# Optimization experiments

Hardware: AMD Instinct MI355X
Metric: run time of the kernel (lower is better)

## Reference

```python
import jax, jax.numpy as jnp
import numpy as np

H = 1024          # hidden_size
NH = 16           # num_attention_heads
HD = H // NH      # attention_head_size = 64
B, S = 8, 1024
LN_EPS = 1e-12


def setup_inputs() -> dict:
    key = jax.random.key(0)
    ks = jax.random.split(key, 12)
    sc = 0.02
    return {
        "input_tensor": jax.random.normal(ks[0], (B, S, H), dtype=jnp.float32),
        "attention_mask": jnp.zeros((B, S), dtype=jnp.float32),
        # LinearMem params (quantization disabled -> plain Linear, torch layout [out,in])
        "Wq": jax.random.normal(ks[1], (H, H), dtype=jnp.float32) * sc,
        "bq": jnp.zeros((H,), dtype=jnp.float32),
        "Wk": jax.random.normal(ks[2], (H, H), dtype=jnp.float32) * sc,
        "bk": jnp.zeros((H,), dtype=jnp.float32),
        "Wv": jax.random.normal(ks[3], (H, H), dtype=jnp.float32) * sc,
        "bv": jnp.zeros((H,), dtype=jnp.float32),
        "Wo": jax.random.normal(ks[4], (H, H), dtype=jnp.float32) * sc,
        "bo": jnp.zeros((H,), dtype=jnp.float32),
        "ln_gamma": jnp.ones((H,), dtype=jnp.float32),
        "ln_beta": jnp.zeros((H,), dtype=jnp.float32),
    }


def _heads(x):  # [B,S,H] -> [B,NH,S,HD]
    return x.reshape(B, S, NH, HD).transpose(0, 2, 1, 3)


def reference(input_tensor, attention_mask, Wq, bq, Wk, bk, Wv, bv, Wo, bo, ln_gamma, ln_beta):
    # Q/K/V projections (LinearMem with quantization disabled == Linear)
    q = _heads(jnp.einsum('bsh,oh->bso', input_tensor, Wq) + bq)
    k = _heads(jnp.einsum('bsh,oh->bso', input_tensor, Wk) + bk)
    v = _heads(jnp.einsum('bsh,oh->bso', input_tensor, Wv) + bv)
    scores = jnp.einsum('bnqd,bnkd->bnqk', q, k) / np.float32(np.sqrt(HD))
    scores = scores + attention_mask[:, None, None, :]  # additive mask [B,1,1,S]
    probs = jax.nn.softmax(scores, axis=-1)  # dropout = identity in eval
    ctx = jnp.einsum('bnqk,bnkd->bnqd', probs, v)
    ctx = ctx.transpose(0, 2, 1, 3).reshape(B, S, H)
    # output projection + residual LayerNorm (eps=1e-12)
    out = jnp.einsum('bsh,oh->bso', ctx, Wo) + bo
    resid = out + input_tensor
    mu = jnp.mean(resid, axis=-1, keepdims=True)
    var = jnp.mean(jnp.square(resid - mu), axis=-1, keepdims=True)
    return (resid - mu) * jax.lax.rsqrt(var + LN_EPS) * ln_gamma + ln_beta
```

## Files before the change

### kernel.cpp

```cpp
#include <hip/hip_runtime.h>

#define NHh 16

typedef unsigned short ushortT;
typedef __attribute__((ext_vector_type(8))) short short8;
typedef __attribute__((ext_vector_type(4))) float floatx4;

__device__ __forceinline__ ushortT f2bf(float x) {
    union { float f; unsigned int u; } cv; cv.f = x;
    unsigned int u = cv.u;
    unsigned int r = u + 0x7fffu + ((u >> 16) & 1u);
    return (ushortT)(r >> 16);
}

__device__ __forceinline__ unsigned pack2_trunc(float a, float b) {
    union { float f; unsigned u; } ua, ub;
    ua.f = a; ub.f = b;
    return (ub.u & 0xffff0000u) | (ua.u >> 16);
}

__device__ __forceinline__ void gload_lds16(const ushortT* g, ushortT* l) {
    __builtin_amdgcn_global_load_lds(
        (const __attribute__((address_space(1))) void*)g,
        (__attribute__((address_space(3))) void*)l, 16, 0, 0);
}

__global__ __launch_bounds__(256) void cvt_all(const float* __restrict__ x,
        const float* __restrict__ W0, const float* __restrict__ W1,
        const float* __restrict__ W2, const float* __restrict__ W3,
        ushortT* __restrict__ Xb, ushortT* __restrict__ Wall, ushortT* __restrict__ Wob) {
    int bid = blockIdx.x;
    const float* in; ushortT* out; int i;
    if (bid < 8192) {
        in = x; out = Xb; i = bid * 256 + threadIdx.x;
    } else {
        int z = (bid - 8192) >> 10;
        in = (z == 0) ? W0 : (z == 1) ? W1 : (z == 2) ? W2 : W3;
        out = (z < 3) ? (Wall + (size_t)z * 1048576) : Wob;
        i = ((bid - 8192) & 1023) * 256 + threadIdx.x;
    }
    float4 f = ((const float4*)in)[i];
    uint2 o;
    o.x = (unsigned)f2bf(f.x) | ((unsigned)f2bf(f.y) << 16);
    o.y = (unsigned)f2bf(f.z) | ((unsigned)f2bf(f.w) << 16);
    ((uint2*)out)[i] = o;
}

__global__ __launch_bounds__(512, 1) void qkv_pipe(
        const ushortT* __restrict__ X, const ushortT* __restrict__ Wall,
        const float* __restrict__ b0, const float* __restrict__ b1, const float* __restrict__ b2,
        ushortT* __restrict__ Qo, ushortT* __restrict__ Ko, ushortT* __restrict__ Vo) {
    __shared__ __align__(16) ushortT As[2 * 16384];
    __shared__ __align__(16) ushortT Bs[2 * 12288];

    const int l = blockIdx.x;
    const int xcd = l & 7;
    const int j = l >> 3;
    const int mg = j >> 4;
    const int nt = j & 15;
    const int arow0 = (mg * 8 + xcd) * 256;
    const int brow0 = nt * 192;

    const int tid = threadIdx.x;
    const int lane = tid & 63;
    const int w = tid >> 6;
    const int wr = w >> 2;
    const int wc = w & 3;
    const int qd = lane >> 4, ln = lane & 15;

    const ushortT* srcA[4]; const ushortT* srcB[3];
    int oA[4], oB[3];
#pragma unroll
    for (int k = 0; k < 4; k++) {
        int o = k * 8192 + tid * 16;
        int rowblk = o >> 11, ks = (o >> 10) & 1, r = (o >> 6) & 15;
        int c2 = ((o >> 4) & 3) ^ ((r >> 3) << 1);
        srcA[k] = X + (size_t)(arow0 + rowblk * 16 + r) * 1024 + ks * 32 + c2 * 8;
        oA[k] = o;
    }
#pragma unroll
    for (int k = 0; k < 3; k++) {
        int o = k * 8192 + tid * 16;
        int rowblk = o >> 11, ks = (o >> 10) & 1, r = (o >> 6) & 15;
        int c2 = ((o >> 4) & 3) ^ ((r >> 3) << 1);
        srcB[k] = Wall + (size_t)(brow0 + rowblk * 16 + r) * 1024 + ks * 32 + c2 * 8;
        oB[k] = o;
    }

    floatx4 acc[8][3];
#pragma unroll
    for (int i = 0; i < 8; i++)
#pragma unroll
        for (int jj = 0; jj < 3; jj++) acc[i][jj] = (floatx4){0.f, 0.f, 0.f, 0.f};

    auto STAGE = [&](int buf) {
#pragma unroll
        for (int k = 0; k < 4; k++) {
            gload_lds16(srcA[k], (ushortT*)((char*)As + buf * 32768 + oA[k]));
            srcA[k] += 64;
        }
#pragma unroll
        for (int k = 0; k < 3; k++) {
            gload_lds16(srcB[k], (ushortT*)((char*)Bs + buf * 24576 + oB[k]));
            srcB[k] += 64;
        }
    };

    const int lnc = ln * 64 + ((qd ^ ((ln >> 3) << 1)) * 16);

    short8 a0[8], bf0[3], a1[8], bf1[3];

    auto RD = [&](short8 (&af)[8], short8 (&bf)[3], const char* Ab, const char* Bb, int ksb) {
#pragma unroll
        for (int mi = 0; mi < 8; mi++)
            af[mi] = *(const short8*)(Ab + (wr * 8 + mi) * 2048 + ksb + lnc);
#pragma unroll
        for (int ni = 0; ni < 3; ni++)
            bf[ni] = *(const short8*)(Bb + (wc * 3 + ni) * 2048 + ksb + lnc);
    };
    auto MM = [&](short8 (&af)[8], short8 (&bf)[3]) {
        __builtin_amdgcn_s_setprio(1);
#pragma unroll
        for (int mi = 0; mi < 8; mi++)
#pragma unroll
            for (int ni = 0; ni < 3; ni++)
                acc[mi][ni] = __builtin_amdgcn_mfma_f32_16x16x32_bf16(af[mi], bf[ni], acc[mi][ni], 0, 0, 0);
        __builtin_amdgcn_s_setprio(0);
    };

    STAGE(0); STAGE(1);
    asm volatile("s_waitcnt vmcnt(7)" ::: "memory");
    __builtin_amdgcn_s_barrier();
    RD(a0, bf0, (const char*)As, (const char*)Bs, 0);
    asm volatile("s_waitcnt lgkmcnt(0)" ::: "memory");
    __builtin_amdgcn_sched_barrier(0);

    for (int T = 0; T < 16; T++) {
        const char* Ab = (const char*)As + (T & 1) * 32768;
        const char* Bb = (const char*)Bs + (T & 1) * 24576;
        const char* An = (const char*)As + ((T + 1) & 1) * 32768;
        const char* Bn = (const char*)Bs + ((T + 1) & 1) * 24576;
        RD(a1, bf1, Ab, Bb, 1024);
        __builtin_amdgcn_sched_barrier(0);
        MM(a0, bf0);
        asm volatile("s_waitcnt lgkmcnt(0)" ::: "memory");
        asm volatile("s_waitcnt vmcnt(0)" ::: "memory");
        __builtin_amdgcn_sched_barrier(0);
        __builtin_amdgcn_s_barrier();
        if (T < 14) STAGE(T & 1);
        if (T < 15) RD(a0, bf0, An, Bn, 0);
        __builtin_amdgcn_sched_barrier(0);
        MM(a1, bf1);
        asm volatile("s_waitcnt lgkmcnt(0)" ::: "memory");
        __builtin_amdgcn_sched_barrier(0);
    }

#pragma unroll
    for (int ni = 0; ni < 3; ni++) {
        int n = brow0 + wc * 48 + ni * 16 + ln;
        int z = n >> 10;
        int col = n & 1023;
        int h = col >> 6, d = col & 63;
        const float* bias = (z == 0) ? b0 : (z == 1) ? b1 : b2;
        float bb = bias[col];
        if (z == 2) {
#pragma unroll
            for (int mi = 0; mi < 8; mi++) {
                int m = arow0 + wr * 128 + mi * 16 + qd * 4;
                int b = m >> 10, s = m & 1023;
                ushort4 pk;
                pk.x = f2bf(acc[mi][ni][0] + bb);
                pk.y = f2bf(acc[mi][ni][1] + bb);
                pk.z = f2bf(acc[mi][ni][2] + bb);
                pk.w = f2bf(acc[mi][ni][3] + bb);
                *(ushort4*)&Vo[((size_t)(b * NHh + h) * 64 + d) * 1024 + s] = pk;
            }
        } else {
            ushortT* Out = z ? Ko : Qo;
#pragma unroll
            for (int mi = 0; mi < 8; mi++) {
#pragma unroll
                for (int r2 = 0; r2 < 4; r2++) {
                    int m = arow0 + wr * 128 + mi * 16 + qd * 4 + r2;
                    int b = m >> 10, s = m & 1023;
                    Out[(size_t)((b * NHh + h) * 1024 + s) * 64 + d] =
                        f2bf(acc[mi][ni][r2] + bb);
                }
            }
        }
    }
}

__device__ __forceinline__ void gemm_core_256x128(
        const ushortT* __restrict__ Ap, const ushortT* __restrict__ Bp,
        int arow0, int brow0, ushortT* As3, ushortT* Bs3,
        int tid, int wr, int wc, int qd, int ln, floatx4 (&acc)[4][4]) {
    const ushortT* srcA[4]; const ushortT* srcB[2];
    int oA[4], oB[2];
#pragma unroll
    for (int k = 0; k < 4; k++) {
        int o = k * 8192 + tid * 16;
        int rowblk = o >> 11, ks = (o >> 10) & 1, r = (o >> 6) & 15;
        int c2 = ((o >> 4) & 3) ^ ((r >> 3) << 1);
        srcA[k] = Ap + (size_t)(arow0 + rowblk * 16 + r) * 1024 + ks * 32 + c2 * 8;
        oA[k] = o;
    }
#pragma unroll
    for (int k = 0; k < 2; k++) {
        int o = k * 8192 + tid * 16;
        int rowblk = o >> 11, ks = (o >> 10) & 1, r = (o >> 6) & 15;
        int c2 = ((o >> 4) & 3) ^ ((r >> 3) << 1);
        srcB[k] = Bp + (size_t)(brow0 + rowblk * 16 + r) * 1024 + ks * 32 + c2 * 8;
        oB[k] = o;
    }
#pragma unroll
    for (int t = 0; t < 2; t++) {
#pragma unroll
        for (int k = 0; k < 4; k++) {
            gload_lds16(srcA[k], (ushortT*)((char*)As3 + t * 32768 + oA[k]));
            srcA[k] += 64;
        }
#pragma unroll
        for (int k = 0; k < 2; k++) {
            gload_lds16(srcB[k], (ushortT*)((char*)Bs3 + t * 16384 + oB[k]));
            srcB[k] += 64;
        }
    }
    asm volatile("s_waitcnt vmcnt(6)" ::: "memory");
    __builtin_amdgcn_s_barrier();

    const int lnc = ln * 64 + ((qd ^ ((ln >> 3) << 1)) * 16);

    int bi = 0, si = 2;
    for (int T = 0; T < 16; T++) {
        const char* Ab = (const char*)As3 + bi * 32768;
        const char* Bb = (const char*)Bs3 + bi * 16384;
        short8 afr[4][2], bfr[4][2];
#pragma unroll
        for (int mi = 0; mi < 4; mi++)
#pragma unroll
            for (int ks = 0; ks < 2; ks++)
                afr[mi][ks] = *(const short8*)(Ab + (mi * 4 + wr) * 2048 + ks * 1024 + lnc);
#pragma unroll
        for (int ni = 0; ni < 4; ni++)
#pragma unroll
            for (int ks = 0; ks < 2; ks++)
                bfr[ni][ks] = *(const short8*)(Bb + (ni * 2 + wc) * 2048 + ks * 1024 + lnc);
        if (T < 14) {
#pragma unroll
            for (int k = 0; k < 4; k++) {
                gload_lds16(srcA[k], (ushortT*)((char*)As3 + si * 32768 + oA[k]));
                srcA[k] += 64;
            }
#pragma unroll
            for (int k = 0; k < 2; k++) {
                gload_lds16(srcB[k], (ushortT*)((char*)Bs3 + si * 16384 + oB[k]));
                srcB[k] += 64;
            }
        }
        __builtin_amdgcn_s_barrier();
        asm volatile("s_waitcnt lgkmcnt(0)" ::: "memory");
        __builtin_amdgcn_sched_barrier(0);
        __builtin_amdgcn_s_setprio(1);
#pragma unroll
        for (int mi = 0; mi < 4; mi++)
#pragma unroll
            for (int ni = 0; ni < 4; ni++)
#pragma unroll
                for (int ks = 0; ks < 2; ks++)
                    acc[mi][ni] = __builtin_amdgcn_mfma_f32_16x16x32_bf16(
                        afr[mi][ks], bfr[ni][ks], acc[mi][ni], 0, 0, 0);
        __builtin_amdgcn_s_setprio(0);
        if (T < 14) { asm volatile("s_waitcnt vmcnt(6)" ::: "memory"); }
        else        { asm volatile("s_waitcnt vmcnt(0)" ::: "memory"); }
        __builtin_amdgcn_s_barrier();
        bi = (bi == 2) ? 0 : bi + 1;
        si = (si == 2) ? 0 : si + 1;
    }
}

__global__ __launch_bounds__(512, 1) void oproj_gemm3(const ushortT* __restrict__ A,
        const ushortT* __restrict__ Wt, const float* __restrict__ bias,
        const float* __restrict__ Xf, float* __restrict__ Pj) {
    __shared__ __align__(16) ushortT As3[3 * 16384];
    __shared__ __align__(16) ushortT Bs3[3 * 8192];

    const int l = blockIdx.x;
    const int xcd = l & 7;
    const int j = l >> 3;
    const int tid = threadIdx.x;
    const int lane = tid & 63;
    const int w = tid >> 6;
    const int wr = w >> 1, wc = w & 1;
    const int qd = lane >> 4, ln = lane & 15;

    const int arow0 = ((j & 3) * 8 + xcd) * 256;
    const int brow0 = (j >> 2) * 128;

    floatx4 acc[4][4];
#pragma unroll
    for (int i = 0; i < 4; i++)
#pragma unroll
        for (int jj = 0; jj < 4; jj++) acc[i][jj] = (floatx4){0.f, 0.f, 0.f, 0.f};

    gemm_core_256x128(A, Wt, arow0, brow0, As3, Bs3, tid, wr, wc, qd, ln, acc);

#pragma unroll
    for (int ni = 0; ni < 4; ni++) {
        int n = brow0 + ni * 32 + wc * 16 + ln;
        float bb = bias[n];
#pragma unroll
        for (int mi = 0; mi < 4; mi++) {
#pragma unroll
            for (int r2 = 0; r2 < 4; r2++) {
                int m = arow0 + mi * 64 + wr * 16 + qd * 4 + r2;
                Pj[(size_t)m * 1024 + n] = acc[mi][ni][r2] + bb + Xf[(size_t)m * 1024 + n];
            }
        }
    }
}

__global__ __launch_bounds__(512, 4) void attn8(const ushortT* __restrict__ Q,
        const ushortT* __restrict__ K, const ushortT* __restrict__ Vg_t,
        const float* __restrict__ mask, ushortT* __restrict__ ctx) {
    __shared__ __align__(16) ushortT Ks[128 * 64];
    __shared__ __align__(16) ushortT Vt[64 * 128];
    __shared__ __align__(16) ushortT Ps[8][32 * 36];

    const int tid = threadIdx.x;
    const int lane = tid & 63;
    const int w = tid >> 6;
    const int qd = lane >> 4;
    const int ln = lane & 15;
    const int l = blockIdx.x;
    const int bh = l & 127;
    const int b = bh >> 4;
    const int h = bh & 15;
    const int qb = l >> 7;

    const ushortT* Qg = Q + (size_t)bh * 65536;
    const ushortT* Kg = K + (size_t)bh * 65536;
    const ushortT* Vg = Vg_t + (size_t)bh * 65536;
    const float* mrow = mask + b * 1024;
    const float LOG2E = 1.4426950408889634f;
    const float SCL = 0.125f * 1.4426950408889634f;

    short8 qf[2][2];
#pragma unroll
    for (int g = 0; g < 2; g++)
#pragma unroll
        for (int ks = 0; ks < 2; ks++)
            qf[g][ks] = *(const short8*)(Qg + (size_t)(qb * 256 + w * 32 + g * 16 + ln) * 64 + ks * 32 + qd * 8);

    float lst[2] = {0.f, 0.f};
    floatx4 accO[2][4];
#pragma unroll
    for (int g = 0; g < 2; g++)
#pragma unroll
        for (int j = 0; j < 4; j++) accO[g][j] = (floatx4){0.f, 0.f, 0.f, 0.f};

    const int ksr = lane >> 3;
    const int kc  = lane & 7;
    const int vdr = lane >> 4;
    const int vcc = lane & 15;

    for (int kt = 0; kt < 8; ++kt) {
        __syncthreads();

#pragma unroll
        for (int ii = 0; ii < 2; ii++) {
            int i = w * 2 + ii;
            int srow = i * 8 + ksr;
            gload_lds16(Kg + (size_t)(kt * 128 + srow) * 64 + (kc ^ ksr) * 8,
                        Ks + i * 512 + lane * 8);
        }
#pragma unroll
        for (int ii = 0; ii < 2; ii++) {
            int i = w * 2 + ii;
            int d = i * 4 + vdr;
            gload_lds16(Vg + (size_t)d * 1024 + kt * 128 + (vcc ^ (d & 15)) * 8,
                        Vt + i * 512 + lane * 8);
        }

        __syncthreads();

#pragma unroll
        for (int h2 = 0; h2 < 2; ++h2) {
#pragma unroll
            for (int mip = 0; mip < 2; ++mip) {
                floatx4 sv[2][2];
#pragma unroll
                for (int mi2 = 0; mi2 < 2; mi2++)
#pragma unroll
                    for (int g = 0; g < 2; g++) sv[mi2][g] = (floatx4){0.f, 0.f, 0.f, 0.f};
#pragma unroll
                for (int ks = 0; ks < 2; ks++) {
                    short8 af[2];
#pragma unroll
                    for (int mi2 = 0; mi2 < 2; mi2++)
                        af[mi2] = *(const short8*)&Ks[(h2 * 64 + mip * 32 + mi2 * 16 + ln) * 64 +
                                                      (((ks * 4 + qd) ^ (ln & 7)) * 8)];
#pragma unroll
                    for (int mi2 = 0; mi2 < 2; mi2++)
#pragma unroll
                        for (int g = 0; g < 2; g++)
                            sv[mi2][g] = __builtin_amdgcn_mfma_f32_16x16x32_bf16(af[mi2], qf[g][ks], sv[mi2][g], 0, 0, 0);
                }

#pragma unroll
                for (int mi2 = 0; mi2 < 2; mi2++) {
                    floatx4 m4 = *(const floatx4*)(mrow + kt * 128 + h2 * 64 + mip * 32 + mi2 * 16 + qd * 4);
                    floatx4 mm;
                    mm[0] = m4[0] * LOG2E; mm[1] = m4[1] * LOG2E;
                    mm[2] = m4[2] * LOG2E; mm[3] = m4[3] * LOG2E;
#pragma unroll
                    for (int g = 0; g < 2; g++) {
                        float p0 = __builtin_amdgcn_exp2f(sv[mi2][g][0] * SCL + mm[0]);
                        float p1 = __builtin_amdgcn_exp2f(sv[mi2][g][1] * SCL + mm[1]);
                        float p2 = __builtin_amdgcn_exp2f(sv[mi2][g][2] * SCL + mm[2]);
                        float p3 = __builtin_amdgcn_exp2f(sv[mi2][g][3] * SCL + mm[3]);
                        lst[g] += (p0 + p1) + (p2 + p3);
                        uint2 wv;
                        wv.x = pack2_trunc(p0, p1);
                        wv.y = pack2_trunc(p2, p3);
                        *(uint2*)&Ps[w][(g * 16 + ln) * 36 + mi2 * 16 + qd * 4] = wv;
                    }
                }

                short8 ap[2], bv[4];
#pragma unroll
                for (int g = 0; g < 2; g++)
                    ap[g] = *(const short8*)&Ps[w][(g * 16 + ln) * 36 + qd * 8];
#pragma unroll
                for (int j = 0; j < 4; j++)
                    bv[j] = *(const short8*)&Vt[(j * 16 + ln) * 128 +
                                                (((h2 * 8 + mip * 4 + qd) ^ ln) * 8)];
#pragma unroll
                for (int g = 0; g < 2; g++)
#pragma unroll
                    for (int j = 0; j < 4; j++)
                        accO[g][j] = __builtin_amdgcn_mfma_f32_16x16x32_bf16(ap[g], bv[j], accO[g][j], 0, 0, 0);
            }
        }
    }

#pragma unroll
    for (int g = 0; g < 2; g++) {
        lst[g] += __shfl_xor(lst[g], 16, 64);
        lst[g] += __shfl_xor(lst[g], 32, 64);
    }

#pragma unroll
    for (int g = 0; g < 2; g++) {
#pragma unroll
        for (int r = 0; r < 4; r++) {
            float lv = __shfl(lst[g], qd * 4 + r, 64);
            float linv = 1.f / lv;
            int q = qb * 256 + w * 32 + g * 16 + qd * 4 + r;
#pragma unroll
            for (int j = 0; j < 4; j++) {
                int d = j * 16 + ln;
                ctx[((size_t)(b * 1024 + q)) * 1024 + h * 64 + d] = f2bf(accO[g][j][r] * linv);
            }
        }
    }
}

__global__ __launch_bounds__(256) void ln_res(const float* __restrict__ Pj,
        const float* __restrict__ gamma, const float* __restrict__ beta, float* __restrict__ out) {
    __shared__ float red[8];
    int row = blockIdx.x;
    int t = threadIdx.x;
    const float4 p4 = ((const float4*)(Pj + (size_t)row * 1024))[t];
    float r0 = p4.x, r1 = p4.y, r2 = p4.z, r3 = p4.w;
    float s = r0 + r1 + r2 + r3;
    float ss = r0 * r0 + r1 * r1 + r2 * r2 + r3 * r3;
#pragma unroll
    for (int o = 1; o < 64; o <<= 1) { s += __shfl_xor(s, o, 64); ss += __shfl_xor(ss, o, 64); }
    int w = t >> 6;
    if ((t & 63) == 0) { red[w] = s; red[4 + w] = ss; }
    __syncthreads();
    s = red[0] + red[1] + red[2] + red[3];
    ss = red[4] + red[5] + red[6] + red[7];
    float mu = s * (1.f / 1024.f);
    float var = ss * (1.f / 1024.f) - mu * mu;
    float inv = rsqrtf(var + 1e-12f);
    const float4 g4 = ((const float4*)gamma)[t];
    const float4 b4 = ((const float4*)beta)[t];
    float4 o4;
    o4.x = (r0 - mu) * inv * g4.x + b4.x;
    o4.y = (r1 - mu) * inv * g4.y + b4.y;
    o4.z = (r2 - mu) * inv * g4.z + b4.z;
    o4.w = (r3 - mu) * inv * g4.w + b4.w;
    ((float4*)(out + (size_t)row * 1024))[t] = o4;
}

extern "C" void kernel_launch(void* const* d_in, const int* in_sizes, int n_in,
                              void* d_out, int out_size, void* d_ws, size_t ws_size,
                              hipStream_t stream) {
    const float* x     = (const float*)d_in[0];
    const float* mask  = (const float*)d_in[1];
    const float* Wq    = (const float*)d_in[2];
    const float* bq    = (const float*)d_in[3];
    const float* Wk    = (const float*)d_in[4];
    const float* bk    = (const float*)d_in[5];
    const float* Wv    = (const float*)d_in[6];
    const float* bv    = (const float*)d_in[7];
    const float* Wo    = (const float*)d_in[8];
    const float* bo    = (const float*)d_in[9];
    const float* gamma = (const float*)d_in[10];
    const float* beta  = (const float*)d_in[11];
    float* out = (float*)d_out;

    char* ws = (char*)d_ws;
    ushortT* Xb   = (ushortT*)(ws);
    ushortT* Wall = (ushortT*)(ws + (16u << 20));
    ushortT* Wob  = (ushortT*)(ws + (22u << 20));
    ushortT* Qb   = (ushortT*)(ws + (24u << 20));
    ushortT* Kb   = (ushortT*)(ws + (40u << 20));
    ushortT* Vb   = (ushortT*)(ws + (56u << 20));
    ushortT* Cb   = (ushortT*)(ws);
    float*   Pj   = (float*)(ws + (24u << 20));

    cvt_all<<<12288, 256, 0, stream>>>(x, Wq, Wk, Wv, Wo, Xb, Wall, Wob);
    qkv_pipe<<<512, 512, 0, stream>>>(Xb, Wall, bq, bk, bv, Qb, Kb, Vb);
    attn8<<<512, 512, 0, stream>>>(Qb, Kb, Vb, mask, Cb);
    oproj_gemm3<<<256, 512, 0, stream>>>(Cb, Wob, bo, x, Pj);
    ln_res<<<8192, 256, 0, stream>>>(Pj, gamma, beta, out);
}
```

Measured before the change: 267.9 us.

## Use 16-wave blocks for QKV and output-projection GEMMs with simpler double buffering

Both GEMM kernels move from 8 waves of 512 threads to 16 waves of 1024 threads. Each wave computes a smaller sub-tile, which cuts accumulators and fragment registers per wave and spreads the tile loads across more threads. The software-pipelined register double buffering (and the triple-buffered LDS in the output projection) is replaced by a plain two-stage LDS pipeline that waits for all loads every K step. This trades explicit instruction-level overlap for more waves per CU to hide latency. The launch_bounds min-blocks value of 4 at 1024 threads may not be achievable, and the tighter barrier and wait pattern could stall more often.

After: 264.4 us. Within noise of the previous version (-1.3%).

```diff
diff --git a/kernel.cpp b/kernel.cpp
--- a/kernel.cpp
+++ b/kernel.cpp
@@ -46,7 +46,7 @@
     ((uint2*)out)[i] = o;
 }
 
-__global__ __launch_bounds__(512, 1) void qkv_pipe(
+__global__ __launch_bounds__(1024, 4) void qkv16(
         const ushortT* __restrict__ X, const ushortT* __restrict__ Wall,
         const float* __restrict__ b0, const float* __restrict__ b1, const float* __restrict__ b2,
         ushortT* __restrict__ Qo, ushortT* __restrict__ Ko, ushortT* __restrict__ Vo) {
@@ -68,91 +68,76 @@
     const int wc = w & 3;
     const int qd = lane >> 4, ln = lane & 15;
 
-    const ushortT* srcA[4]; const ushortT* srcB[3];
-    int oA[4], oB[3];
-#pragma unroll
-    for (int k = 0; k < 4; k++) {
-        int o = k * 8192 + tid * 16;
+    const ushortT* srcA[2]; int oA[2];
+#pragma unroll
+    for (int k = 0; k < 2; k++) {
+        int o = k * 16384 + tid * 16;
         int rowblk = o >> 11, ks = (o >> 10) & 1, r = (o >> 6) & 15;
         int c2 = ((o >> 4) & 3) ^ ((r >> 3) << 1);
         srcA[k] = X + (size_t)(arow0 + rowblk * 16 + r) * 1024 + ks * 32 + c2 * 8;
         oA[k] = o;
     }
-#pragma unroll
-    for (int k = 0; k < 3; k++) {
-        int o = k * 8192 + tid * 16;
+    const ushortT* srcB[2]; int oB[2];
+#pragma unroll
+    for (int k = 0; k < 2; k++) {
+        int o = k * 16384 + tid * 16;
         int rowblk = o >> 11, ks = (o >> 10) & 1, r = (o >> 6) & 15;
         int c2 = ((o >> 4) & 3) ^ ((r >> 3) << 1);
         srcB[k] = Wall + (size_t)(brow0 + rowblk * 16 + r) * 1024 + ks * 32 + c2 * 8;
         oB[k] = o;
     }
 
-    floatx4 acc[8][3];
-#pragma unroll
-    for (int i = 0; i < 8; i++)
+    floatx4 acc[4][3];
+#pragma unroll
+    for (int i = 0; i < 4; i++)
 #pragma unroll
         for (int jj = 0; jj < 3; jj++) acc[i][jj] = (floatx4){0.f, 0.f, 0.f, 0.f};
 
     auto STAGE = [&](int buf) {
 #pragma unroll
-        for (int k = 0; k < 4; k++) {
+        for (int k = 0; k < 2; k++) {
             gload_lds16(srcA[k], (ushortT*)((char*)As + buf * 32768 + oA[k]));
             srcA[k] += 64;
         }
-#pragma unroll
-        for (int k = 0; k < 3; k++) {
-            gload_lds16(srcB[k], (ushortT*)((char*)Bs + buf * 24576 + oB[k]));
-            srcB[k] += 64;
+        gload_lds16(srcB[0], (ushortT*)((char*)Bs + buf * 24576 + oB[0]));
+        srcB[0] += 64;
+        if (tid < 512) {
+            gload_lds16(srcB[1], (ushortT*)((char*)Bs + buf * 24576 + oB[1]));
+            srcB[1] += 64;
         }
     };
 
     const int lnc = ln * 64 + ((qd ^ ((ln >> 3) << 1)) * 16);
 
-    short8 a0[8], bf0[3], a1[8], bf1[3];
-
-    auto RD = [&](short8 (&af)[8], short8 (&bf)[3], const char* Ab, const char* Bb, int ksb) {
-#pragma unroll
-        for (int mi = 0; mi < 8; mi++)
-            af[mi] = *(const short8*)(Ab + (wr * 8 + mi) * 2048 + ksb + lnc);
-#pragma unroll
-        for (int ni = 0; ni < 3; ni++)
-            bf[ni] = *(const short8*)(Bb + (wc * 3 + ni) * 2048 + ksb + lnc);
-    };
-    auto MM = [&](short8 (&af)[8], short8 (&bf)[3]) {
-        __builtin_amdgcn_s_setprio(1);
-#pragma unroll
-        for (int mi = 0; mi < 8; mi++)
-#pragma unroll
-            for (int ni = 0; ni < 3; ni++)
-                acc[mi][ni] = __builtin_amdgcn_mfma_f32_16x16x32_bf16(af[mi], bf[ni], acc[mi][ni], 0, 0, 0);
-        __builtin_amdgcn_s_setprio(0);
-    };
-
-    STAGE(0); STAGE(1);
-    asm volatile("s_waitcnt vmcnt(7)" ::: "memory");
+    STAGE(0);
+    asm volatile("s_waitcnt vmcnt(0)" ::: "memory");
     __builtin_amdgcn_s_barrier();
-    RD(a0, bf0, (const char*)As, (const char*)Bs, 0);
-    asm volatile("s_waitcnt lgkmcnt(0)" ::: "memory");
-    __builtin_amdgcn_sched_barrier(0);
 
     for (int T = 0; T < 16; T++) {
         const char* Ab = (const char*)As + (T & 1) * 32768;
         const char* Bb = (const char*)Bs + (T & 1) * 24576;
-        const char* An = (const char*)As + ((T + 1) & 1) * 32768;
-        const char* Bn = (const char*)Bs + ((T + 1) & 1) * 24576;
-        RD(a1, bf1, Ab, Bb, 1024);
-        __builtin_amdgcn_sched_barrier(0);
-        MM(a0, bf0);
-        asm volatile("s_waitcnt lgkmcnt(0)" ::: "memory");
+        if (T < 15) STAGE((T + 1) & 1);
+        short8 af[4], bf[3];
+#pragma unroll
+        for (int ks = 0; ks < 2; ks++) {
+#pragma unroll
+            for (int mi = 0; mi < 4; mi++)
+                af[mi] = *(const short8*)(Ab + (wr * 4 + mi) * 2048 + ks * 1024 + lnc);
+#pragma unroll
+            for (int ni = 0; ni < 3; ni++)
+                bf[ni] = *(const short8*)(Bb + (wc * 3 + ni) * 2048 + ks * 1024 + lnc);
+            asm volatile("s_waitcnt lgkmcnt(0)" ::: "memory");
+            __builtin_amdgcn_sched_barrier(0);
+            __builtin_amdgcn_s_setprio(1);
+#pragma unroll
+            for (int mi = 0; mi < 4; mi++)
+#pragma unroll
+                for (int ni = 0; ni < 3; ni++)
+                    acc[mi][ni] = __builtin_amdgcn_mfma_f32_16x16x32_bf16(af[mi], bf[ni], acc[mi][ni], 0, 0, 0);
+            __builtin_amdgcn_s_setprio(0);
+        }
         asm volatile("s_waitcnt vmcnt(0)" ::: "memory");
-        __builtin_amdgcn_sched_barrier(0);
         __builtin_amdgcn_s_barrier();
-        if (T < 14) STAGE(T & 1);
-        if (T < 15) RD(a0, bf0, An, Bn, 0);
-        __builtin_amdgcn_sched_barrier(0);
-        MM(a1, bf1);
-        asm volatile("s_waitcnt lgkmcnt(0)" ::: "memory");
-        __builtin_amdgcn_sched_barrier(0);
     }
 
 #pragma unroll
@@ -165,8 +150,8 @@
         float bb = bias[col];
         if (z == 2) {
 #pragma unroll
-            for (int mi = 0; mi < 8; mi++) {
-                int m = arow0 + wr * 128 + mi * 16 + qd * 4;
+            for (int mi = 0; mi < 4; mi++) {
+                int m = arow0 + wr * 64 + mi * 16 + qd * 4;
                 int b = m >> 10, s = m & 1023;
                 ushort4 pk;
                 pk.x = f2bf(acc[mi][ni][0] + bb);
@@ -178,10 +163,10 @@
         } else {
             ushortT* Out = z ? Ko : Qo;
 #pragma unroll
-            for (int mi = 0; mi < 8; mi++) {
+            for (int mi = 0; mi < 4; mi++) {
 #pragma unroll
                 for (int r2 = 0; r2 < 4; r2++) {
-                    int m = arow0 + wr * 128 + mi * 16 + qd * 4 + r2;
+                    int m = arow0 + wr * 64 + mi * 16 + qd * 4 + r2;
                     int b = m >> 10, s = m & 1023;
                     Out[(size_t)((b * NHh + h) * 1024 + s) * 64 + d] =
                         f2bf(acc[mi][ni][r2] + bb);
@@ -191,99 +176,11 @@
     }
 }
 
-__device__ __forceinline__ void gemm_core_256x128(
-        const ushortT* __restrict__ Ap, const ushortT* __restrict__ Bp,
-        int arow0, int brow0, ushortT* As3, ushortT* Bs3,
-        int tid, int wr, int wc, int qd, int ln, floatx4 (&acc)[4][4]) {
-    const ushortT* srcA[4]; const ushortT* srcB[2];
-    int oA[4], oB[2];
-#pragma unroll
-    for (int k = 0; k < 4; k++) {
-        int o = k * 8192 + tid * 16;
-        int rowblk = o >> 11, ks = (o >> 10) & 1, r = (o >> 6) & 15;
-        int c2 = ((o >> 4) & 3) ^ ((r >> 3) << 1);
-        srcA[k] = Ap + (size_t)(arow0 + rowblk * 16 + r) * 1024 + ks * 32 + c2 * 8;
-        oA[k] = o;
-    }
-#pragma unroll
-    for (int k = 0; k < 2; k++) {
-        int o = k * 8192 + tid * 16;
-        int rowblk = o >> 11, ks = (o >> 10) & 1, r = (o >> 6) & 15;
-        int c2 = ((o >> 4) & 3) ^ ((r >> 3) << 1);
-        srcB[k] = Bp + (size_t)(brow0 + rowblk * 16 + r) * 1024 + ks * 32 + c2 * 8;
-        oB[k] = o;
-    }
-#pragma unroll
-    for (int t = 0; t < 2; t++) {
-#pragma unroll
-        for (int k = 0; k < 4; k++) {
-            gload_lds16(srcA[k], (ushortT*)((char*)As3 + t * 32768 + oA[k]));
-            srcA[k] += 64;
-        }
-#pragma unroll
-        for (int k = 0; k < 2; k++) {
-            gload_lds16(srcB[k], (ushortT*)((char*)Bs3 + t * 16384 + oB[k]));
-            srcB[k] += 64;
-        }
-    }
-    asm volatile("s_waitcnt vmcnt(6)" ::: "memory");
-    __builtin_amdgcn_s_barrier();
-
-    const int lnc = ln * 64 + ((qd ^ ((ln >> 3) << 1)) * 16);
-
-    int bi = 0, si = 2;
-    for (int T = 0; T < 16; T++) {
-        const char* Ab = (const char*)As3 + bi * 32768;
-        const char* Bb = (const char*)Bs3 + bi * 16384;
-        short8 afr[4][2], bfr[4][2];
-#pragma unroll
-        for (int mi = 0; mi < 4; mi++)
-#pragma unroll
-            for (int ks = 0; ks < 2; ks++)
-                afr[mi][ks] = *(const short8*)(Ab + (mi * 4 + wr) * 2048 + ks * 1024 + lnc);
-#pragma unroll
-        for (int ni = 0; ni < 4; ni++)
-#pragma unroll
-            for (int ks = 0; ks < 2; ks++)
-                bfr[ni][ks] = *(const short8*)(Bb + (ni * 2 + wc) * 2048 + ks * 1024 + lnc);
-        if (T < 14) {
-#pragma unroll
-            for (int k = 0; k < 4; k++) {
-                gload_lds16(srcA[k], (ushortT*)((char*)As3 + si * 32768 + oA[k]));
-                srcA[k] += 64;
-            }
-#pragma unroll
-            for (int k = 0; k < 2; k++) {
-                gload_lds16(srcB[k], (ushortT*)((char*)Bs3 + si * 16384 + oB[k]));
-                srcB[k] += 64;
-            }
-        }
-        __builtin_amdgcn_s_barrier();
-        asm volatile("s_waitcnt lgkmcnt(0)" ::: "memory");
-        __builtin_amdgcn_sched_barrier(0);
-        __builtin_amdgcn_s_setprio(1);
-#pragma unroll
-        for (int mi = 0; mi < 4; mi++)
-#pragma unroll
-            for (int ni = 0; ni < 4; ni++)
-#pragma unroll
-                for (int ks = 0; ks < 2; ks++)
-                    acc[mi][ni] = __builtin_amdgcn_mfma_f32_16x16x32_bf16(
-                        afr[mi][ks], bfr[ni][ks], acc[mi][ni], 0, 0, 0);
-        __builtin_amdgcn_s_setprio(0);
-        if (T < 14) { asm volatile("s_waitcnt vmcnt(6)" ::: "memory"); }
-        else        { asm volatile("s_waitcnt vmcnt(0)" ::: "memory"); }
-        __builtin_amdgcn_s_barrier();
-        bi = (bi == 2) ? 0 : bi + 1;
-        si = (si == 2) ? 0 : si + 1;
-    }
-}
-
-__global__ __launch_bounds__(512, 1) void oproj_gemm3(const ushortT* __restrict__ A,
+__global__ __launch_bounds__(1024, 4) void oproj16(const ushortT* __restrict__ A,
         const ushortT* __restrict__ Wt, const float* __restrict__ bias,
         const float* __restrict__ Xf, float* __restrict__ Pj) {
-    __shared__ __align__(16) ushortT As3[3 * 16384];
-    __shared__ __align__(16) ushortT Bs3[3 * 8192];
+    __shared__ __align__(16) ushortT As[2 * 16384];
+    __shared__ __align__(16) ushortT Bs[2 * 8192];
 
     const int l = blockIdx.x;
     const int xcd = l & 7;
@@ -291,29 +188,88 @@
     const int tid = threadIdx.x;
     const int lane = tid & 63;
     const int w = tid >> 6;
-    const int wr = w >> 1, wc = w & 1;
+    const int wr = w >> 2, wc = w & 3;
     const int qd = lane >> 4, ln = lane & 15;
 
     const int arow0 = ((j & 3) * 8 + xcd) * 256;
     const int brow0 = (j >> 2) * 128;
 
-    floatx4 acc[4][4];
+    const ushortT* srcA[2]; int oA[2];
+#pragma unroll
+    for (int k = 0; k < 2; k++) {
+        int o = k * 16384 + tid * 16;
+        int rowblk = o >> 11, ks = (o >> 10) & 1, r = (o >> 6) & 15;
+        int c2 = ((o >> 4) & 3) ^ ((r >> 3) << 1);
+        srcA[k] = A + (size_t)(arow0 + rowblk * 16 + r) * 1024 + ks * 32 + c2 * 8;
+        oA[k] = o;
+    }
+    const ushortT* srcB0; int oB0;
+    {
+        int o = tid * 16;
+        int rowblk = o >> 11, ks = (o >> 10) & 1, r = (o >> 6) & 15;
+        int c2 = ((o >> 4) & 3) ^ ((r >> 3) << 1);
+        srcB0 = Wt + (size_t)(brow0 + rowblk * 16 + r) * 1024 + ks * 32 + c2 * 8;
+        oB0 = o;
+    }
+
+    floatx4 acc[4][2];
 #pragma unroll
     for (int i = 0; i < 4; i++)
 #pragma unroll
-        for (int jj = 0; jj < 4; jj++) acc[i][jj] = (floatx4){0.f, 0.f, 0.f, 0.f};
-
-    gemm_core_256x128(A, Wt, arow0, brow0, As3, Bs3, tid, wr, wc, qd, ln, acc);
-
-#pragma unroll
-    for (int ni = 0; ni < 4; ni++) {
-        int n = brow0 + ni * 32 + wc * 16 + ln;
+        for (int jj = 0; jj < 2; jj++) acc[i][jj] = (floatx4){0.f, 0.f, 0.f, 0.f};
+
+    auto STAGE = [&](int buf) {
+#pragma unroll
+        for (int k = 0; k < 2; k++) {
+            gload_lds16(srcA[k], (ushortT*)((char*)As + buf * 32768 + oA[k]));
+            srcA[k] += 64;
+        }
+        gload_lds16(srcB0, (ushortT*)((char*)Bs + buf * 16384 + oB0));
+        srcB0 += 64;
+    };
+
+    const int lnc = ln * 64 + ((qd ^ ((ln >> 3) << 1)) * 16);
+
+    STAGE(0);
+    asm volatile("s_waitcnt vmcnt(0)" ::: "memory");
+    __builtin_amdgcn_s_barrier();
+
+    for (int T = 0; T < 16; T++) {
+        const char* Ab = (const char*)As + (T & 1) * 32768;
+        const char* Bb = (const char*)Bs + (T & 1) * 16384;
+        if (T < 15) STAGE((T + 1) & 1);
+        short8 af[4], bf[2];
+#pragma unroll
+        for (int ks = 0; ks < 2; ks++) {
+#pragma unroll
+            for (int mi = 0; mi < 4; mi++)
+                af[mi] = *(const short8*)(Ab + (wr * 4 + mi) * 2048 + ks * 1024 + lnc);
+#pragma unroll
+            for (int ni = 0; ni < 2; ni++)
+                bf[ni] = *(const short8*)(Bb + (wc * 2 + ni) * 2048 + ks * 1024 + lnc);
+            asm volatile("s_waitcnt lgkmcnt(0)" ::: "memory");
+            __builtin_amdgcn_sched_barrier(0);
+            __builtin_amdgcn_s_setprio(1);
+#pragma unroll
+            for (int mi = 0; mi < 4; mi++)
+#pragma unroll
+                for (int ni = 0; ni < 2; ni++)
+                    acc[mi][ni] = __builtin_amdgcn_mfma_f32_16x16x32_bf16(af[mi], bf[ni], acc[mi][ni], 0, 0, 0);
+            __builtin_amdgcn_s_setprio(0);
+        }
+        asm volatile("s_waitcnt vmcnt(0)" ::: "memory");
+        __builtin_amdgcn_s_barrier();
+    }
+
+#pragma unroll
+    for (int ni = 0; ni < 2; ni++) {
+        int n = brow0 + wc * 32 + ni * 16 + ln;
         float bb = bias[n];
 #pragma unroll
         for (int mi = 0; mi < 4; mi++) {
 #pragma unroll
             for (int r2 = 0; r2 < 4; r2++) {
-                int m = arow0 + mi * 64 + wr * 16 + qd * 4 + r2;
+                int m = arow0 + wr * 64 + mi * 16 + qd * 4 + r2;
                 Pj[(size_t)m * 1024 + n] = acc[mi][ni][r2] + bb + Xf[(size_t)m * 1024 + n];
             }
         }
@@ -523,8 +479,8 @@
     float*   Pj   = (float*)(ws + (24u << 20));
 
     cvt_all<<<12288, 256, 0, stream>>>(x, Wq, Wk, Wv, Wo, Xb, Wall, Wob);
-    qkv_pipe<<<512, 512, 0, stream>>>(Xb, Wall, bq, bk, bv, Qb, Kb, Vb);
+    qkv16<<<512, 1024, 0, stream>>>(Xb, Wall, bq, bk, bv, Qb, Kb, Vb);
     attn8<<<512, 512, 0, stream>>>(Qb, Kb, Vb, mask, Cb);
-    oproj_gemm3<<<256, 512, 0, stream>>>(Cb, Wob, bo, x, Pj);
+    oproj16<<<256, 1024, 0, stream>>>(Cb, Wob, bo, x, Pj);
     ln_res<<<8192, 256, 0, stream>>>(Pj, gamma, beta, out);
 }
```
